# Kernel tuning notes

Hardware: AMD Instinct MI355X
Metric: run time of the kernel (lower is better)

Reference implementation:

```python
import jax, jax.numpy as jnp
import numpy as np

IN_SLICE = (4, 4)   # input bit-plane widths, MSB first
W_SLICE = (4, 4)    # weight bit-plane widths, MSB first
KSIZE, STRIDE, PAD = 3, 1, 1
B, CIN, COUT, H, W = 16, 64, 128, 32, 32


def _slice_planes(x, bits):
    """Dynamic fixed-point quantization to sum(bits) signed bits, then split
    the magnitude into bit-planes (sign folded into each plane). Exact:
    sum_i 2**shift_i * plane_i == q, and scale * q ~= x."""
    n = int(sum(bits))
    qmax = float(2 ** (n - 1) - 1)
    scale = jnp.max(jnp.abs(x)) / qmax
    q = jnp.clip(jnp.round(x / scale), -qmax, qmax)
    sgn = jnp.sign(q)
    u = jnp.abs(q)
    planes, shifts = [], []
    s = n
    for b in bits:
        s -= b
        planes.append(sgn * (jnp.floor(u / (2.0 ** s)) % (2.0 ** b)))
        shifts.append(s)
    return planes, shifts, scale


def _unfold(x, k, stride, pad):
    """torch.nn.functional.unfold, (C, kh, kw) channel-major ordering.
    Returns [B, L, C*k*k], Ho, Wo."""
    b, c, h, w = x.shape
    xp = jnp.pad(x, ((0, 0), (0, 0), (pad, pad), (pad, pad)))
    ho = (h + 2 * pad - k) // stride + 1
    wo = (w + 2 * pad - k) // stride + 1
    cols = []
    for kh in range(k):
        for kw in range(k):
            cols.append(xp[:, :, kh:kh + (ho - 1) * stride + 1:stride,
                            kw:kw + (wo - 1) * stride + 1:stride])
    patches = jnp.stack(cols, axis=2)              # [B, C, k*k, Ho, Wo]
    patches = patches.reshape(b, c * k * k, ho * wo)
    return patches.transpose(0, 2, 1), ho, wo      # [B, L, K]


def _mem_conv(input, weight, bias):
    cout = weight.shape[0]
    wm = weight.reshape(cout, -1).T                # [K, Cout], matches weight.reshape(Cout,-1).t()
    xun, ho, wo = _unfold(input, KSIZE, STRIDE, PAD)
    xplanes, xshifts, xscale = _slice_planes(xun, IN_SLICE)
    wplanes, wshifts, wscale = _slice_planes(wm, W_SLICE)
    acc = jnp.zeros((input.shape[0], xun.shape[1], cout), dtype=input.dtype)
    for xp, sx in zip(xplanes, xshifts):
        for wp, sw in zip(wplanes, wshifts):
            # low-precision bit-plane GEMM with power-of-two shift recombination
            acc = acc + (2.0 ** (sx + sw)) * jnp.einsum('blk,ko->blo', xp, wp)
    out = (xscale * wscale) * acc                  # [B, L, Cout]
    out = out.transpose(0, 2, 1).reshape(input.shape[0], cout, ho, wo)
    return out + bias[None, :, None, None]


def setup_inputs() -> dict:
    key = jax.random.key(0)
    k1, k2, k3 = jax.random.split(key, 3)
    x = jax.random.normal(k1, (B, CIN, H, W), dtype=jnp.float32)
    fan_in = CIN * KSIZE * KSIZE
    bound = 1.0 / np.sqrt(fan_in)  # kaiming_uniform(a=sqrt(5)) -> U(-1/sqrt(fan_in), +)
    weight = jax.random.uniform(k2, (COUT, CIN, KSIZE, KSIZE), dtype=jnp.float32,
                                minval=-bound, maxval=bound)
    bias = jax.random.uniform(k3, (COUT,), dtype=jnp.float32, minval=-bound, maxval=bound)
    return {"input": x, "weight": weight, "bias": bias}


def reference(input, weight, bias):
    return _mem_conv(input, weight, bias)
```

## Files before the change

kernel.cpp:

```cpp
#include <hip/hip_runtime.h>

#define B_    16
#define CIN   64
#define COUT  128
#define H_    32
#define W_    32
#define HP    34
#define XROW  2176
#define NPB   256

typedef __attribute__((ext_vector_type(8)))  short  short8;
typedef __attribute__((ext_vector_type(16))) float  float16v;

__device__ __forceinline__ unsigned short f2bf(float q) {
  return (unsigned short)(__builtin_bit_cast(unsigned int, q) >> 16);
}

__device__ __forceinline__ float wave_max256(const float* __restrict__ p) {
  const int lane = threadIdx.x & 63;
  float m = fmaxf(fmaxf(p[lane], p[lane + 64]),
                  fmaxf(p[lane + 128], p[lane + 192]));
#pragma unroll
  for (int off = 32; off > 0; off >>= 1)
    m = fmaxf(m, __shfl_down(m, off, 64));
  return __shfl(m, 0, 64);
}

__global__ __launch_bounds__(256) void maxabs_kernel(
    const float4* __restrict__ x4, const float4* __restrict__ w4,
    float* __restrict__ bmx, float* __restrict__ bmw) {
  const int nx4 = B_ * CIN * H_ * W_ / 4;
  const int nw4 = COUT * CIN * 9 / 4;
  const int tid = blockIdx.x * 256 + threadIdx.x;
  const int stride = NPB * 256;
  float mx = 0.0f, mw = 0.0f;
#pragma unroll
  for (int k = 0; k < 4; ++k) {
    float4 v = x4[tid + k * stride];
    mx = fmaxf(mx, fmaxf(fmaxf(fabsf(v.x), fabsf(v.y)),
                         fmaxf(fabsf(v.z), fabsf(v.w))));
  }
  if (tid < nw4) {
    float4 v = w4[tid];
    mw = fmaxf(mw, fmaxf(fmaxf(fabsf(v.x), fabsf(v.y)),
                         fmaxf(fabsf(v.z), fabsf(v.w))));
  }
#pragma unroll
  for (int off = 32; off > 0; off >>= 1) {
    mx = fmaxf(mx, __shfl_down(mx, off, 64));
    mw = fmaxf(mw, __shfl_down(mw, off, 64));
  }
  __shared__ float smx[4], smw[4];
  const int wid = threadIdx.x >> 6;
  if ((threadIdx.x & 63) == 0) { smx[wid] = mx; smw[wid] = mw; }
  __syncthreads();
  if (threadIdx.x == 0) {
#pragma unroll
    for (int i = 1; i < 4; ++i) { mx = fmaxf(mx, smx[i]); mw = fmaxf(mw, smw[i]); }
    bmx[blockIdx.x] = mx;
    bmw[blockIdx.x] = mw;
  }
}

__global__ __launch_bounds__(256) void quant_pack_kernel(
    const float* __restrict__ x, const float* __restrict__ w,
    const float* __restrict__ bmx, const float* __restrict__ bmw,
    unsigned short* __restrict__ qx, unsigned short* __restrict__ qw) {
  __shared__ __align__(16) unsigned short lds[W_ * 72];
  const int t = threadIdx.x;
  const int bb = blockIdx.x;
  if (bb < 512) {
    const int b = bb >> 5, y = bb & 31;
    const float s = wave_max256(bmx) / 127.0f;
#pragma unroll
    for (int k = 0; k < 8; ++k) {
      const int u = t + k * 256;
      const int cin = u >> 5, xx = u & 31;
      float q = rintf(x[((b * CIN + cin) * H_ + y) * W_ + xx] / s);
      q = fminf(fmaxf(q, -127.0f), 127.0f);
      lds[xx * 72 + cin] = f2bf(q);
    }
    __syncthreads();
    const size_t row = (size_t)(b * HP + y + 1) * XROW;
    for (int c = t; c < 272; c += 256) {
      const int k16 = c / 68;
      const int r   = c - k16 * 68;
      const int kbh = r / 34;
      const int xs  = r - kbh * 34;
      uint4 v; v.x = v.y = v.z = v.w = 0;
      if (xs >= 1 && xs <= 32)
        v = *(const uint4*)(&lds[(xs - 1) * 72 + k16 * 16 + kbh * 8]);
      *(uint4*)(qx + row + (size_t)c * 8) = v;
    }
  } else if (bb < 544) {
    const int idx = bb - 512;
    const int b = idx >> 1, yy = (idx & 1) ? 33 : 0;
    const size_t row = (size_t)(b * HP + yy) * XROW;
    uint4 z; z.x = z.y = z.z = z.w = 0;
    for (int c = t; c < 272; c += 256)
      *(uint4*)(qx + row + (size_t)c * 8) = z;
  } else {
    const int i = (bb - 544) * 256 + t;
    const float s = wave_max256(bmw) / 127.0f;
    float q = rintf(w[i] / s);
    q = fminf(fmaxf(q, -127.0f), 127.0f);
    const int kw = i % 3; int j = i / 3;
    const int kh = j % 3; j /= 3;
    const int c = j & 63; const int o = j >> 6;
    const int sidx = kh * 3 + kw;
    const int k16 = c >> 4, kb2 = (c >> 3) & 1, e = c & 7;
    qw[(size_t)((((sidx * 4 + k16) * 2 + kb2) * 128 + o)) * 8 + e] = f2bf(q);
  }
}

__global__ __launch_bounds__(256, 2) void conv_mfma_kernel(
    const unsigned short* __restrict__ qx,
    const unsigned short* __restrict__ qw,
    const float* __restrict__ bmx, const float* __restrict__ bmw,
    const float* __restrict__ bias, float* __restrict__ out) {
  const int lane = threadIdx.x & 63;
  const int wv   = threadIdx.x >> 6;
  const int col  = lane & 31;
  const int kb   = lane >> 5;
  const int y    = blockIdx.x;
  const int b    = blockIdx.y;
  const int co0  = wv * 32;

  float16v acc0 = (float16v)0.0f, acc1 = (float16v)0.0f;

  const unsigned short* __restrict__ xp =
      qx + (size_t)b * HP * XROW + kb * 272 + col * 8;
  const unsigned short* __restrict__ wp =
      qw + kb * 1024 + (co0 + col) * 8;

#pragma unroll
  for (int kh = 0; kh < 3; ++kh) {
    const unsigned short* __restrict__ xr = xp + (size_t)(y + kh) * XROW;
#pragma unroll
    for (int kw = 0; kw < 3; ++kw) {
      const int s = kh * 3 + kw;
#pragma unroll
      for (int k16 = 0; k16 < 4; ++k16) {
        short8 a  = *(const short8*)(wp + (s * 4 + k16) * 2048);
        short8 bf = *(const short8*)(xr + k16 * 544 + kw * 8);
        if (((s * 4 + k16) & 1) == 0)
          acc0 = __builtin_amdgcn_mfma_f32_32x32x16_bf16(a, bf, acc0, 0, 0, 0);
        else
          acc1 = __builtin_amdgcn_mfma_f32_32x32x16_bf16(a, bf, acc1, 0, 0, 0);
      }
    }
  }

  const float mx = wave_max256(bmx);
  const float mw = wave_max256(bmw);
  const float sc = (mx / 127.0f) * (mw / 127.0f);
  const float16v acc = acc0 + acc1;
#pragma unroll
  for (int r = 0; r < 16; ++r) {
    const int row  = (r & 3) + 8 * (r >> 2) + 4 * kb;
    const int cout = co0 + row;
    out[((b * COUT + cout) << 10) + y * W_ + col] = sc * acc[r] + bias[cout];
  }
}

extern "C" void kernel_launch(void* const* d_in, const int* in_sizes, int n_in,
                              void* d_out, int out_size, void* d_ws, size_t ws_size,
                              hipStream_t stream) {
  const float* x    = (const float*)d_in[0];
  const float* w    = (const float*)d_in[1];
  const float* bias = (const float*)d_in[2];
  float* out = (float*)d_out;

  float* bmx = (float*)d_ws;
  float* bmw = bmx + 256;
  unsigned short* qx = (unsigned short*)((char*)d_ws + 2048);
  unsigned short* qw = qx + (size_t)B_ * HP * XROW;

  maxabs_kernel<<<NPB, 256, 0, stream>>>((const float4*)x, (const float4*)w,
                                         bmx, bmw);
  quant_pack_kernel<<<832, 256, 0, stream>>>(x, w, bmx, bmw, qx, qw);
  conv_mfma_kernel<<<dim3(32, 16), 256, 0, stream>>>(qx, qw, bmx, bmw, bias, out);
}
```

Measured before the change: 75.85 us.

## Fuse input quantization into conv kernel and merge max-abs with weight packing

Removes the separate quant/pack kernel and its padded bf16 input buffer. The conv kernel now quantizes its three input rows straight into LDS, with zero halos. Weight max-abs and weight quantize/pack move into extra blocks of the max-abs kernel, so each of the 32 weight blocks recomputes the full weight max redundantly. This cuts one kernel launch and a global round trip for the quantized input, at the cost of reading each fp32 input row three times across neighbouring conv blocks and an extra barrier.

```diff
diff --git a/kernel.cpp b/kernel.cpp
--- a/kernel.cpp
+++ b/kernel.cpp
@@ -5,9 +5,6 @@
 #define COUT  128
 #define H_    32
 #define W_    32
-#define HP    34
-#define XROW  2176
-#define NPB   256
 
 typedef __attribute__((ext_vector_type(8)))  short  short8;
 typedef __attribute__((ext_vector_type(16))) float  float16v;
@@ -26,123 +23,115 @@
   return __shfl(m, 0, 64);
 }
 
-__global__ __launch_bounds__(256) void maxabs_kernel(
+__global__ __launch_bounds__(256) void prep_kernel(
     const float4* __restrict__ x4, const float4* __restrict__ w4,
-    float* __restrict__ bmx, float* __restrict__ bmw) {
-  const int nx4 = B_ * CIN * H_ * W_ / 4;
-  const int nw4 = COUT * CIN * 9 / 4;
-  const int tid = blockIdx.x * 256 + threadIdx.x;
-  const int stride = NPB * 256;
-  float mx = 0.0f, mw = 0.0f;
+    const float* __restrict__ wflat,
+    float* __restrict__ bmx, float* __restrict__ bmw,
+    unsigned short* __restrict__ qw) {
+  const int t = threadIdx.x;
+  __shared__ float sm[4];
+  if (blockIdx.x < 256) {
+    const int tid = blockIdx.x * 256 + t;
+    float mx = 0.0f;
 #pragma unroll
-  for (int k = 0; k < 4; ++k) {
-    float4 v = x4[tid + k * stride];
-    mx = fmaxf(mx, fmaxf(fmaxf(fabsf(v.x), fabsf(v.y)),
-                         fmaxf(fabsf(v.z), fabsf(v.w))));
-  }
-  if (tid < nw4) {
-    float4 v = w4[tid];
-    mw = fmaxf(mw, fmaxf(fmaxf(fabsf(v.x), fabsf(v.y)),
-                         fmaxf(fabsf(v.z), fabsf(v.w))));
-  }
+    for (int k = 0; k < 4; ++k) {
+      float4 v = x4[tid + k * 65536];
+      mx = fmaxf(mx, fmaxf(fmaxf(fabsf(v.x), fabsf(v.y)),
+                           fmaxf(fabsf(v.z), fabsf(v.w))));
+    }
 #pragma unroll
-  for (int off = 32; off > 0; off >>= 1) {
-    mx = fmaxf(mx, __shfl_down(mx, off, 64));
-    mw = fmaxf(mw, __shfl_down(mw, off, 64));
-  }
-  __shared__ float smx[4], smw[4];
-  const int wid = threadIdx.x >> 6;
-  if ((threadIdx.x & 63) == 0) { smx[wid] = mx; smw[wid] = mw; }
-  __syncthreads();
-  if (threadIdx.x == 0) {
+    for (int off = 32; off > 0; off >>= 1)
+      mx = fmaxf(mx, __shfl_down(mx, off, 64));
+    if ((t & 63) == 0) sm[t >> 6] = mx;
+    __syncthreads();
+    if (t == 0)
+      bmx[blockIdx.x] = fmaxf(fmaxf(sm[0], sm[1]), fmaxf(sm[2], sm[3]));
+  } else {
+    float mw = 0.0f;
+    for (int i = t; i < 18432; i += 256) {
+      float4 v = w4[i];
+      mw = fmaxf(mw, fmaxf(fmaxf(fabsf(v.x), fabsf(v.y)),
+                           fmaxf(fabsf(v.z), fabsf(v.w))));
+    }
 #pragma unroll
-    for (int i = 1; i < 4; ++i) { mx = fmaxf(mx, smx[i]); mw = fmaxf(mw, smw[i]); }
-    bmx[blockIdx.x] = mx;
-    bmw[blockIdx.x] = mw;
-  }
-}
-
-__global__ __launch_bounds__(256) void quant_pack_kernel(
-    const float* __restrict__ x, const float* __restrict__ w,
-    const float* __restrict__ bmx, const float* __restrict__ bmw,
-    unsigned short* __restrict__ qx, unsigned short* __restrict__ qw) {
-  __shared__ __align__(16) unsigned short lds[W_ * 72];
-  const int t = threadIdx.x;
-  const int bb = blockIdx.x;
-  if (bb < 512) {
-    const int b = bb >> 5, y = bb & 31;
-    const float s = wave_max256(bmx) / 127.0f;
+    for (int off = 32; off > 0; off >>= 1)
+      mw = fmaxf(mw, __shfl_down(mw, off, 64));
+    if ((t & 63) == 0) sm[t >> 6] = mw;
+    __syncthreads();
+    const float m = fmaxf(fmaxf(sm[0], sm[1]), fmaxf(sm[2], sm[3]));
+    if (t == 0) bmw[0] = m;
+    const float s = m / 127.0f;
+    const int base = (blockIdx.x - 256) * 2304;
 #pragma unroll
-    for (int k = 0; k < 8; ++k) {
-      const int u = t + k * 256;
-      const int cin = u >> 5, xx = u & 31;
-      float q = rintf(x[((b * CIN + cin) * H_ + y) * W_ + xx] / s);
+    for (int mIt = 0; mIt < 9; ++mIt) {
+      const int i = base + t + mIt * 256;
+      float q = rintf(wflat[i] / s);
       q = fminf(fmaxf(q, -127.0f), 127.0f);
-      lds[xx * 72 + cin] = f2bf(q);
+      const int kw = i % 3; int j = i / 3;
+      const int kh = j % 3; j /= 3;
+      const int c = j & 63; const int o = j >> 6;
+      const int sidx = kh * 3 + kw;
+      const int k16 = c >> 4, kb2 = (c >> 3) & 1, e = c & 7;
+      qw[(size_t)((((sidx * 4 + k16) * 2 + kb2) * 128 + o)) * 8 + e] = f2bf(q);
     }
-    __syncthreads();
-    const size_t row = (size_t)(b * HP + y + 1) * XROW;
-    for (int c = t; c < 272; c += 256) {
-      const int k16 = c / 68;
-      const int r   = c - k16 * 68;
-      const int kbh = r / 34;
-      const int xs  = r - kbh * 34;
-      uint4 v; v.x = v.y = v.z = v.w = 0;
-      if (xs >= 1 && xs <= 32)
-        v = *(const uint4*)(&lds[(xs - 1) * 72 + k16 * 16 + kbh * 8]);
-      *(uint4*)(qx + row + (size_t)c * 8) = v;
-    }
-  } else if (bb < 544) {
-    const int idx = bb - 512;
-    const int b = idx >> 1, yy = (idx & 1) ? 33 : 0;
-    const size_t row = (size_t)(b * HP + yy) * XROW;
-    uint4 z; z.x = z.y = z.z = z.w = 0;
-    for (int c = t; c < 272; c += 256)
-      *(uint4*)(qx + row + (size_t)c * 8) = z;
-  } else {
-    const int i = (bb - 544) * 256 + t;
-    const float s = wave_max256(bmw) / 127.0f;
-    float q = rintf(w[i] / s);
-    q = fminf(fmaxf(q, -127.0f), 127.0f);
-    const int kw = i % 3; int j = i / 3;
-    const int kh = j % 3; j /= 3;
-    const int c = j & 63; const int o = j >> 6;
-    const int sidx = kh * 3 + kw;
-    const int k16 = c >> 4, kb2 = (c >> 3) & 1, e = c & 7;
-    qw[(size_t)((((sidx * 4 + k16) * 2 + kb2) * 128 + o)) * 8 + e] = f2bf(q);
   }
 }
 
 __global__ __launch_bounds__(256, 2) void conv_mfma_kernel(
-    const unsigned short* __restrict__ qx,
+    const float* __restrict__ x,
     const unsigned short* __restrict__ qw,
     const float* __restrict__ bmx, const float* __restrict__ bmw,
     const float* __restrict__ bias, float* __restrict__ out) {
-  const int lane = threadIdx.x & 63;
-  const int wv   = threadIdx.x >> 6;
+  __shared__ __align__(16) unsigned short lds[3 * 272 * 8];
+  const int t    = threadIdx.x;
+  const int lane = t & 63;
+  const int wv   = t >> 6;
   const int col  = lane & 31;
   const int kb   = lane >> 5;
   const int y    = blockIdx.x;
   const int b    = blockIdx.y;
   const int co0  = wv * 32;
 
+  const float mx = wave_max256(bmx);
+  const float sx = mx / 127.0f;
+
+  const int g  = t >> 5;
+  const int xx = t & 31;
+  const int k16w = g >> 1, kbw = g & 1;
+  if (t < 48) {
+    const int r = t >> 4, q2 = t & 15;
+    const int hk = q2 >> 2, hb = (q2 >> 1) & 1, hxs = (q2 & 1) * 33;
+    *(short8*)&lds[(((r * 4 + hk) * 2 + hb) * 34 + hxs) * 8] = (short8)0;
+  }
+#pragma unroll
+  for (int r = 0; r < 3; ++r) {
+    const int yy = y + r - 1;
+    short8 pk = (short8)0;
+    if (yy >= 0 && yy < H_) {
+#pragma unroll
+      for (int j = 0; j < 8; ++j) {
+        const float v = x[((b * CIN + g * 8 + j) * H_ + yy) * W_ + xx];
+        float q = rintf(v / sx);
+        q = fminf(fmaxf(q, -127.0f), 127.0f);
+        pk[j] = (short)f2bf(q);
+      }
+    }
+    *(short8*)&lds[(((r * 4 + k16w) * 2 + kbw) * 34 + (xx + 1)) * 8] = pk;
+  }
+  __syncthreads();
+
   float16v acc0 = (float16v)0.0f, acc1 = (float16v)0.0f;
-
-  const unsigned short* __restrict__ xp =
-      qx + (size_t)b * HP * XROW + kb * 272 + col * 8;
-  const unsigned short* __restrict__ wp =
-      qw + kb * 1024 + (co0 + col) * 8;
-
+  const unsigned short* __restrict__ wp = qw + kb * 1024 + (co0 + col) * 8;
 #pragma unroll
   for (int kh = 0; kh < 3; ++kh) {
-    const unsigned short* __restrict__ xr = xp + (size_t)(y + kh) * XROW;
 #pragma unroll
     for (int kw = 0; kw < 3; ++kw) {
       const int s = kh * 3 + kw;
 #pragma unroll
       for (int k16 = 0; k16 < 4; ++k16) {
         short8 a  = *(const short8*)(wp + (s * 4 + k16) * 2048);
-        short8 bf = *(const short8*)(xr + k16 * 544 + kw * 8);
+        short8 bf = *(const short8*)&lds[(((kh * 4 + k16) * 2 + kb) * 34 +
+                                          col + kw) * 8];
         if (((s * 4 + k16) & 1) == 0)
           acc0 = __builtin_amdgcn_mfma_f32_32x32x16_bf16(a, bf, acc0, 0, 0, 0);
         else
@@ -151,9 +140,7 @@
     }
   }
 
-  const float mx = wave_max256(bmx);
-  const float mw = wave_max256(bmw);
-  const float sc = (mx / 127.0f) * (mw / 127.0f);
+  const float sc = sx * (bmw[0] / 127.0f);
   const float16v acc = acc0 + acc1;
 #pragma unroll
   for (int r = 0; r < 16; ++r) {
@@ -173,11 +160,9 @@
 
   float* bmx = (float*)d_ws;
   float* bmw = bmx + 256;
-  unsigned short* qx = (unsigned short*)((char*)d_ws + 2048);
-  unsigned short* qw = qx + (size_t)B_ * HP * XROW;
+  unsigned short* qw = (unsigned short*)((char*)d_ws + 2048);
 
-  maxabs_kernel<<<NPB, 256, 0, stream>>>((const float4*)x, (const float4*)w,
-                                         bmx, bmw);
-  quant_pack_kernel<<<832, 256, 0, stream>>>(x, w, bmx, bmw, qx, qw);
-  conv_mfma_kernel<<<dim3(32, 16), 256, 0, stream>>>(qx, qw, bmx, bmw, bias, out);
+  prep_kernel<<<288, 256, 0, stream>>>((const float4*)x, (const float4*)w, w,
+                                       bmx, bmw, qw);
+  conv_mfma_kernel<<<dim3(32, 16), 256, 0, stream>>>(x, qw, bmx, bmw, bias, out);
 }
```

After: 82.85 us. +9.2%, slower.

## Fuse max-abs, quantize-pack and MFMA conv into one kernel with atomic grid sync

Applied to the files above, without the earlier changes.

Replaces the three kernel launches (max-abs reduction, quantize/pack, MFMA conv) with a single 576-block kernel. Blocks hand off work through tagged 64-bit atomic flags in workspace: partial maxima are published, one block reduces them and broadcasts the scales, then waits for every pack block before releasing the conv phase. The aim is to remove launch gaps and inter-kernel drains and to spread the weight quantization over fewer, wider blocks. In exchange it depends on all blocks being co-resident, since it spins on flags. The flags are never reset between calls, so on a repeat call stale tags from the previous run can satisfy the polls early.

```diff
diff --git a/kernel.cpp b/kernel.cpp
--- a/kernel.cpp
+++ b/kernel.cpp
@@ -7,71 +7,105 @@
 #define W_    32
 #define HP    34
 #define XROW  2176
-#define NPB   256
 
 typedef __attribute__((ext_vector_type(8)))  short  short8;
 typedef __attribute__((ext_vector_type(16))) float  float16v;
 
+#define MAGTAG 0x7E57C0DEull
+
 __device__ __forceinline__ unsigned short f2bf(float q) {
   return (unsigned short)(__builtin_bit_cast(unsigned int, q) >> 16);
 }
 
-__device__ __forceinline__ float wave_max256(const float* __restrict__ p) {
-  const int lane = threadIdx.x & 63;
-  float m = fmaxf(fmaxf(p[lane], p[lane + 64]),
-                  fmaxf(p[lane + 128], p[lane + 192]));
+__device__ __forceinline__ void pub(unsigned long long* p, unsigned int v) {
+  __hip_atomic_exchange(p, (MAGTAG << 32) | (unsigned long long)v,
+                        __ATOMIC_RELEASE, __HIP_MEMORY_SCOPE_AGENT);
+}
+__device__ __forceinline__ unsigned int pollv(unsigned long long* p) {
+  unsigned long long v =
+      __hip_atomic_load(p, __ATOMIC_ACQUIRE, __HIP_MEMORY_SCOPE_AGENT);
+  while ((v >> 32) != MAGTAG) {
+    __builtin_amdgcn_s_sleep(2);
+    v = __hip_atomic_load(p, __ATOMIC_ACQUIRE, __HIP_MEMORY_SCOPE_AGENT);
+  }
+  return (unsigned int)v;
+}
+
+__device__ __forceinline__ float max4(float4 v) {
+  return fmaxf(fmaxf(fabsf(v.x), fabsf(v.y)), fmaxf(fabsf(v.z), fabsf(v.w)));
+}
+
+__device__ __forceinline__ float blk_max(float m, int t, volatile float* sred) {
 #pragma unroll
   for (int off = 32; off > 0; off >>= 1)
     m = fmaxf(m, __shfl_down(m, off, 64));
-  return __shfl(m, 0, 64);
-}
-
-__global__ __launch_bounds__(256) void maxabs_kernel(
-    const float4* __restrict__ x4, const float4* __restrict__ w4,
-    float* __restrict__ bmx, float* __restrict__ bmw) {
-  const int nx4 = B_ * CIN * H_ * W_ / 4;
-  const int nw4 = COUT * CIN * 9 / 4;
-  const int tid = blockIdx.x * 256 + threadIdx.x;
-  const int stride = NPB * 256;
-  float mx = 0.0f, mw = 0.0f;
-#pragma unroll
-  for (int k = 0; k < 4; ++k) {
-    float4 v = x4[tid + k * stride];
-    mx = fmaxf(mx, fmaxf(fmaxf(fabsf(v.x), fabsf(v.y)),
-                         fmaxf(fabsf(v.z), fabsf(v.w))));
-  }
-  if (tid < nw4) {
-    float4 v = w4[tid];
-    mw = fmaxf(mw, fmaxf(fmaxf(fabsf(v.x), fabsf(v.y)),
-                         fmaxf(fabsf(v.z), fabsf(v.w))));
-  }
-#pragma unroll
-  for (int off = 32; off > 0; off >>= 1) {
-    mx = fmaxf(mx, __shfl_down(mx, off, 64));
-    mw = fmaxf(mw, __shfl_down(mw, off, 64));
-  }
-  __shared__ float smx[4], smw[4];
-  const int wid = threadIdx.x >> 6;
-  if ((threadIdx.x & 63) == 0) { smx[wid] = mx; smw[wid] = mw; }
-  __syncthreads();
-  if (threadIdx.x == 0) {
-#pragma unroll
-    for (int i = 1; i < 4; ++i) { mx = fmaxf(mx, smx[i]); mw = fmaxf(mw, smw[i]); }
-    bmx[blockIdx.x] = mx;
-    bmw[blockIdx.x] = mw;
-  }
-}
-
-__global__ __launch_bounds__(256) void quant_pack_kernel(
+  if ((t & 63) == 0) sred[t >> 6] = m;
+  __syncthreads();
+  const float r = fmaxf(fmaxf(sred[0], sred[1]), fmaxf(sred[2], sred[3]));
+  __syncthreads();
+  return r;
+}
+
+__global__ __launch_bounds__(256, 4) void mega_kernel(
     const float* __restrict__ x, const float* __restrict__ w,
-    const float* __restrict__ bmx, const float* __restrict__ bmw,
+    const float* __restrict__ bias, float* __restrict__ out,
+    unsigned long long* __restrict__ sync,
     unsigned short* __restrict__ qx, unsigned short* __restrict__ qw) {
-  __shared__ __align__(16) unsigned short lds[W_ * 72];
-  const int t = threadIdx.x;
-  const int bb = blockIdx.x;
-  if (bb < 512) {
-    const int b = bb >> 5, y = bb & 31;
-    const float s = wave_max256(bmx) / 127.0f;
+  __shared__ float sred[4];
+  __shared__ float lsc[2];
+  __shared__ __align__(16) unsigned short lds[32 * 72];
+  const int t   = threadIdx.x;
+  const int bid = blockIdx.x;
+
+  if (bid < 512) {
+    const float4* x4 = (const float4*)x;
+    float m = fmaxf(max4(x4[bid * 512 + t]), max4(x4[bid * 512 + 256 + t]));
+    m = blk_max(m, t, sred);
+    if (t == 0) pub(&sync[bid], __float_as_uint(m));
+  } else if (bid < 544) {
+    const float4* w4 = (const float4*)w;
+    const int base = (bid - 512) * 576;
+    float m = fmaxf(max4(w4[base + t]), max4(w4[base + 256 + t]));
+    if (t < 64) m = fmaxf(m, max4(w4[base + 512 + t]));
+    m = blk_max(m, t, sred);
+    if (t == 0) pub(&sync[bid], __float_as_uint(m));
+  } else {
+    const int j = bid - 544;
+    const int b = j >> 1, yy = (j & 1) ? 33 : 0;
+    const size_t row = (size_t)(b * HP + yy) * XROW;
+    uint4 z; z.x = z.y = z.z = z.w = 0;
+    for (int c = t; c < 272; c += 256)
+      *(uint4*)(qx + row + (size_t)c * 8) = z;
+    __syncthreads();
+    if (t == 0) { __threadfence(); pub(&sync[578 + bid], 0); }
+    if (bid != 575) return;
+    float mx = 0.0f, mw = 0.0f;
+    for (int jj = t; jj < 544; jj += 256) {
+      const float f = __uint_as_float(pollv(&sync[jj]));
+      if (jj < 512) mx = fmaxf(mx, f); else mw = fmaxf(mw, f);
+    }
+    mx = blk_max(mx, t, sred);
+    mw = blk_max(mw, t, sred);
+    if (t == 0) {
+      pub(&sync[576], __float_as_uint(mx));
+      pub(&sync[577], __float_as_uint(mw));
+    }
+    for (int jj = t; jj < 575; jj += 256) (void)pollv(&sync[578 + jj]);
+    __syncthreads();
+    if (t == 0) pub(&sync[1154], 0);
+    return;
+  }
+
+  if (t == 0) {
+    lsc[0] = __uint_as_float(pollv(&sync[576]));
+    lsc[1] = __uint_as_float(pollv(&sync[577]));
+  }
+  __syncthreads();
+  const float mx = lsc[0], mw = lsc[1];
+
+  if (bid < 512) {
+    const int b = bid >> 5, y = bid & 31;
+    const float s = mx / 127.0f;
 #pragma unroll
     for (int k = 0; k < 8; ++k) {
       const int u = t + k * 256;
@@ -92,46 +126,43 @@
         v = *(const uint4*)(&lds[(xs - 1) * 72 + k16 * 16 + kbh * 8]);
       *(uint4*)(qx + row + (size_t)c * 8) = v;
     }
-  } else if (bb < 544) {
-    const int idx = bb - 512;
-    const int b = idx >> 1, yy = (idx & 1) ? 33 : 0;
-    const size_t row = (size_t)(b * HP + yy) * XROW;
-    uint4 z; z.x = z.y = z.z = z.w = 0;
-    for (int c = t; c < 272; c += 256)
-      *(uint4*)(qx + row + (size_t)c * 8) = z;
+    __syncthreads();
+    if (t == 0) { __threadfence(); pub(&sync[578 + bid], 0); }
   } else {
-    const int i = (bb - 544) * 256 + t;
-    const float s = wave_max256(bmw) / 127.0f;
-    float q = rintf(w[i] / s);
-    q = fminf(fmaxf(q, -127.0f), 127.0f);
-    const int kw = i % 3; int j = i / 3;
-    const int kh = j % 3; j /= 3;
-    const int c = j & 63; const int o = j >> 6;
-    const int sidx = kh * 3 + kw;
-    const int k16 = c >> 4, kb2 = (c >> 3) & 1, e = c & 7;
-    qw[(size_t)((((sidx * 4 + k16) * 2 + kb2) * 128 + o)) * 8 + e] = f2bf(q);
-  }
-}
-
-__global__ __launch_bounds__(256, 2) void conv_mfma_kernel(
-    const unsigned short* __restrict__ qx,
-    const unsigned short* __restrict__ qw,
-    const float* __restrict__ bmx, const float* __restrict__ bmw,
-    const float* __restrict__ bias, float* __restrict__ out) {
-  const int lane = threadIdx.x & 63;
-  const int wv   = threadIdx.x >> 6;
+    const float s = mw / 127.0f;
+    const int base = (bid - 512) * 2304;
+#pragma unroll
+    for (int mIt = 0; mIt < 9; ++mIt) {
+      const int i = base + t + mIt * 256;
+      float q = rintf(w[i] / s);
+      q = fminf(fmaxf(q, -127.0f), 127.0f);
+      const int kw = i % 3; int j2 = i / 3;
+      const int kh = j2 % 3; j2 /= 3;
+      const int c = j2 & 63; const int o = j2 >> 6;
+      const int sidx = kh * 3 + kw;
+      const int k16 = c >> 4, kb2 = (c >> 3) & 1, e = c & 7;
+      qw[(size_t)(((sidx * 4 + k16) * 2 + kb2) * 128 + o) * 8 + e] = f2bf(q);
+    }
+    __syncthreads();
+    if (t == 0) { __threadfence(); pub(&sync[578 + bid], 0); }
+    return;
+  }
+
+  if (t == 0) (void)pollv(&sync[1154]);
+  __syncthreads();
+
+  const int lane = t & 63;
+  const int wv   = t >> 6;
   const int col  = lane & 31;
   const int kb   = lane >> 5;
-  const int y    = blockIdx.x;
-  const int b    = blockIdx.y;
+  const int y    = bid & 31;
+  const int b    = bid >> 5;
   const int co0  = wv * 32;
 
   float16v acc0 = (float16v)0.0f, acc1 = (float16v)0.0f;
-
   const unsigned short* __restrict__ xp =
       qx + (size_t)b * HP * XROW + kb * 272 + col * 8;
-  const unsigned short* __restrict__ wp =
-      qw + kb * 1024 + (co0 + col) * 8;
+  const unsigned short* __restrict__ wp = qw + kb * 1024 + (co0 + col) * 8;
 
 #pragma unroll
   for (int kh = 0; kh < 3; ++kh) {
@@ -151,8 +182,6 @@
     }
   }
 
-  const float mx = wave_max256(bmx);
-  const float mw = wave_max256(bmw);
   const float sc = (mx / 127.0f) * (mw / 127.0f);
   const float16v acc = acc0 + acc1;
 #pragma unroll
@@ -171,13 +200,9 @@
   const float* bias = (const float*)d_in[2];
   float* out = (float*)d_out;
 
-  float* bmx = (float*)d_ws;
-  float* bmw = bmx + 256;
-  unsigned short* qx = (unsigned short*)((char*)d_ws + 2048);
+  unsigned long long* syncp = (unsigned long long*)d_ws;
+  unsigned short* qx = (unsigned short*)((char*)d_ws + 16384);
   unsigned short* qw = qx + (size_t)B_ * HP * XROW;
 
-  maxabs_kernel<<<NPB, 256, 0, stream>>>((const float4*)x, (const float4*)w,
-                                         bmx, bmw);
-  quant_pack_kernel<<<832, 256, 0, stream>>>(x, w, bmx, bmw, qx, qw);
-  conv_mfma_kernel<<<dim3(32, 16), 256, 0, stream>>>(qx, qw, bmx, bmw, bias, out);
-}
+  mega_kernel<<<576, 256, 0, stream>>>(x, w, bias, out, syncp, qx, qw);
+}
```

After: 218.5 us. 2.88x slower.

## Switch quantized conv GEMM from bf16 MFMA to int8 MFMA

Applied to the files above, without the earlier changes.

Stores the quantized activations and weights as int8 instead of bf16 and uses the 32x32x32 int8 MFMA with int32 accumulation. This halves the bytes written and read for the packed operands and halves the number of MFMA instructions per output tile. Every value lies in [-127,127], so the int8 path stays exact and the int32 accumulators are converted to float only at the end. The packed layouts and the indexing in the pack and conv kernels are reworked to match the new 32-element K chunks.

```diff
diff --git a/kernel.cpp b/kernel.cpp
--- a/kernel.cpp
+++ b/kernel.cpp
@@ -6,15 +6,11 @@
 #define H_    32
 #define W_    32
 #define HP    34
-#define XROW  2176
+#define XCH   136
 #define NPB   256
 
-typedef __attribute__((ext_vector_type(8)))  short  short8;
-typedef __attribute__((ext_vector_type(16))) float  float16v;
-
-__device__ __forceinline__ unsigned short f2bf(float q) {
-  return (unsigned short)(__builtin_bit_cast(unsigned int, q) >> 16);
-}
+typedef __attribute__((ext_vector_type(4)))  int int4v;
+typedef __attribute__((ext_vector_type(16))) int int16v;
 
 __device__ __forceinline__ float wave_max256(const float* __restrict__ p) {
   const int lane = threadIdx.x & 63;
@@ -29,14 +25,12 @@
 __global__ __launch_bounds__(256) void maxabs_kernel(
     const float4* __restrict__ x4, const float4* __restrict__ w4,
     float* __restrict__ bmx, float* __restrict__ bmw) {
-  const int nx4 = B_ * CIN * H_ * W_ / 4;
   const int nw4 = COUT * CIN * 9 / 4;
   const int tid = blockIdx.x * 256 + threadIdx.x;
-  const int stride = NPB * 256;
   float mx = 0.0f, mw = 0.0f;
 #pragma unroll
   for (int k = 0; k < 4; ++k) {
-    float4 v = x4[tid + k * stride];
+    float4 v = x4[tid + k * 65536];
     mx = fmaxf(mx, fmaxf(fmaxf(fabsf(v.x), fabsf(v.y)),
                          fmaxf(fabsf(v.z), fabsf(v.w))));
   }
@@ -65,8 +59,8 @@
 __global__ __launch_bounds__(256) void quant_pack_kernel(
     const float* __restrict__ x, const float* __restrict__ w,
     const float* __restrict__ bmx, const float* __restrict__ bmw,
-    unsigned short* __restrict__ qx, unsigned short* __restrict__ qw) {
-  __shared__ __align__(16) unsigned short lds[W_ * 72];
+    char* __restrict__ qx, char* __restrict__ qw) {
+  __shared__ __align__(16) char lds[W_ * 80];
   const int t = threadIdx.x;
   const int bb = blockIdx.x;
   if (bb < 512) {
@@ -78,27 +72,26 @@
       const int cin = u >> 5, xx = u & 31;
       float q = rintf(x[((b * CIN + cin) * H_ + y) * W_ + xx] / s);
       q = fminf(fmaxf(q, -127.0f), 127.0f);
-      lds[xx * 72 + cin] = f2bf(q);
+      lds[xx * 80 + cin] = (char)(int)q;
     }
     __syncthreads();
-    const size_t row = (size_t)(b * HP + y + 1) * XROW;
-    for (int c = t; c < 272; c += 256) {
-      const int k16 = c / 68;
-      const int r   = c - k16 * 68;
-      const int kbh = r / 34;
-      const int xs  = r - kbh * 34;
+    char* row = qx + (size_t)(b * HP + y + 1) * (XCH * 16);
+    if (t < XCH) {
+      const int c32 = t / 68;
+      const int r   = t - c32 * 68;
+      const int kb  = r / 34;
+      const int xs  = r - kb * 34;
       uint4 v; v.x = v.y = v.z = v.w = 0;
       if (xs >= 1 && xs <= 32)
-        v = *(const uint4*)(&lds[(xs - 1) * 72 + k16 * 16 + kbh * 8]);
-      *(uint4*)(qx + row + (size_t)c * 8) = v;
+        v = *(const uint4*)(&lds[(xs - 1) * 80 + c32 * 32 + kb * 16]);
+      *(uint4*)(row + t * 16) = v;
     }
   } else if (bb < 544) {
     const int idx = bb - 512;
     const int b = idx >> 1, yy = (idx & 1) ? 33 : 0;
-    const size_t row = (size_t)(b * HP + yy) * XROW;
+    char* row = qx + (size_t)(b * HP + yy) * (XCH * 16);
     uint4 z; z.x = z.y = z.z = z.w = 0;
-    for (int c = t; c < 272; c += 256)
-      *(uint4*)(qx + row + (size_t)c * 8) = z;
+    if (t < XCH) *(uint4*)(row + t * 16) = z;
   } else {
     const int i = (bb - 544) * 256 + t;
     const float s = wave_max256(bmw) / 127.0f;
@@ -108,14 +101,14 @@
     const int kh = j % 3; j /= 3;
     const int c = j & 63; const int o = j >> 6;
     const int sidx = kh * 3 + kw;
-    const int k16 = c >> 4, kb2 = (c >> 3) & 1, e = c & 7;
-    qw[(size_t)((((sidx * 4 + k16) * 2 + kb2) * 128 + o)) * 8 + e] = f2bf(q);
+    const int c32 = c >> 5, kb = (c >> 4) & 1, e = c & 15;
+    qw[(size_t)(((sidx * 2 + c32) * 2 + kb) * 128 + o) * 16 + e] = (char)(int)q;
   }
 }
 
 __global__ __launch_bounds__(256, 2) void conv_mfma_kernel(
-    const unsigned short* __restrict__ qx,
-    const unsigned short* __restrict__ qw,
+    const char* __restrict__ qx,
+    const char* __restrict__ qw,
     const float* __restrict__ bmx, const float* __restrict__ bmw,
     const float* __restrict__ bias, float* __restrict__ out) {
   const int lane = threadIdx.x & 63;
@@ -126,27 +119,25 @@
   const int b    = blockIdx.y;
   const int co0  = wv * 32;
 
-  float16v acc0 = (float16v)0.0f, acc1 = (float16v)0.0f;
+  int16v acc0 = (int16v)0, acc1 = (int16v)0;
 
-  const unsigned short* __restrict__ xp =
-      qx + (size_t)b * HP * XROW + kb * 272 + col * 8;
-  const unsigned short* __restrict__ wp =
-      qw + kb * 1024 + (co0 + col) * 8;
+  const char* __restrict__ xp = qx + ((size_t)(b * HP + y) * 4 + kb) * 544 + col * 16;
+  const char* __restrict__ wp = qw + (kb * 128 + co0 + col) * 16;
 
 #pragma unroll
   for (int kh = 0; kh < 3; ++kh) {
-    const unsigned short* __restrict__ xr = xp + (size_t)(y + kh) * XROW;
+    const char* __restrict__ xr = xp + (size_t)kh * (4 * 544);
 #pragma unroll
     for (int kw = 0; kw < 3; ++kw) {
       const int s = kh * 3 + kw;
 #pragma unroll
-      for (int k16 = 0; k16 < 4; ++k16) {
-        short8 a  = *(const short8*)(wp + (s * 4 + k16) * 2048);
-        short8 bf = *(const short8*)(xr + k16 * 544 + kw * 8);
-        if (((s * 4 + k16) & 1) == 0)
-          acc0 = __builtin_amdgcn_mfma_f32_32x32x16_bf16(a, bf, acc0, 0, 0, 0);
+      for (int c32 = 0; c32 < 2; ++c32) {
+        int4v a  = *(const int4v*)(wp + (s * 2 + c32) * 4096);
+        int4v bf = *(const int4v*)(xr + c32 * 1088 + kw * 16);
+        if (((s * 2 + c32) & 1) == 0)
+          acc0 = __builtin_amdgcn_mfma_i32_32x32x32_i8(a, bf, acc0, 0, 0, 0);
         else
-          acc1 = __builtin_amdgcn_mfma_f32_32x32x16_bf16(a, bf, acc1, 0, 0, 0);
+          acc1 = __builtin_amdgcn_mfma_i32_32x32x32_i8(a, bf, acc1, 0, 0, 0);
       }
     }
   }
@@ -154,12 +145,12 @@
   const float mx = wave_max256(bmx);
   const float mw = wave_max256(bmw);
   const float sc = (mx / 127.0f) * (mw / 127.0f);
-  const float16v acc = acc0 + acc1;
 #pragma unroll
   for (int r = 0; r < 16; ++r) {
     const int row  = (r & 3) + 8 * (r >> 2) + 4 * kb;
     const int cout = co0 + row;
-    out[((b * COUT + cout) << 10) + y * W_ + col] = sc * acc[r] + bias[cout];
+    out[((b * COUT + cout) << 10) + y * W_ + col] =
+        sc * (float)(acc0[r] + acc1[r]) + bias[cout];
   }
 }
 
@@ -173,8 +164,8 @@
 
   float* bmx = (float*)d_ws;
   float* bmw = bmx + 256;
-  unsigned short* qx = (unsigned short*)((char*)d_ws + 2048);
-  unsigned short* qw = qx + (size_t)B_ * HP * XROW;
+  char* qx = (char*)d_ws + 2048;
+  char* qw = qx + (size_t)B_ * HP * XCH * 16;
 
   maxabs_kernel<<<NPB, 256, 0, stream>>>((const float4*)x, (const float4*)w,
                                          bmx, bmw);
```

After: 68.43 us. -9.8%, faster.
